# Kernel tuning notes

Measured on AMD Instinct MI355X. Metric: run time of the kernel, lower is better.

The kernel has to match this reference:

```python
import jax, jax.numpy as jnp
import numpy as np

N = 200000
H = 64
ARITIES = [2, 2, 3]
TUPLES = [300000, 300000, 200000]  # flat idx lengths = tuples * arity = 600000 each


def _linear_params(key, out_f, in_f, scale=0.05):
    kw, kb = jax.random.split(key)
    w = jax.random.normal(kw, (out_f, in_f), jnp.float32) * scale
    b = jax.random.normal(kb, (out_f,), jnp.float32) * scale
    return w, b


def setup_inputs() -> dict:
    key = jax.random.key(0)
    keys = jax.random.split(key, 16)
    inp = {}
    inp["node_states"] = jax.random.normal(keys[0], (N, H), jnp.float32)
    for r, (a, t) in enumerate(zip(ARITIES, TUPLES)):
        inp[f"rel{r}_idx"] = jax.random.randint(keys[1 + r], (t * a,), 0, N, jnp.int64)
    k = 4
    for r, a in enumerate(ARITIES):
        d = a * H
        w1, b1 = _linear_params(keys[k], d, d); k += 1
        w2, b2 = _linear_params(keys[k], d, d); k += 1
        inp[f"r{r}_w1"], inp[f"r{r}_b1"] = w1, b1
        inp[f"r{r}_w2"], inp[f"r{r}_b2"] = w2, b2
    inp["u_w1"], inp["u_b1"] = _linear_params(keys[k], 2 * H, 2 * H); k += 1
    inp["u_w2"], inp["u_b2"] = _linear_params(keys[k], H, 2 * H)
    return inp


def _forward(node_states, idxs, rel_params, u_w1, u_b1, u_w2, u_b2):
    outputs = []
    max_outputs = []
    for idx, a, (w1, b1, w2, b2) in zip(idxs, ARITIES, rel_params):
        # gather node rows, group by tuple: [T, a*H]
        x = node_states[idx].reshape(-1, a * H)
        h = jax.nn.relu(x @ w1.T + b1)
        o = (h @ w2.T + b2).reshape(-1, H)  # [T*a, H] message per participating node
        max_outputs.append(jnp.max(o))
        outputs.append((o, idx))
    max_offset = jnp.max(jnp.stack(max_outputs))
    exps_sum = jnp.full_like(node_states, 1e-16)
    for o, idx in outputs:
        exps_sum = exps_sum.at[idx].add(jnp.exp(8.0 * (o - max_offset)))
    max_msg = (1.0 / 8.0) * jnp.log(exps_sum) + max_offset  # smooth-max LSE
    cat = jnp.concatenate([max_msg, node_states], axis=1)
    h = jax.nn.relu(cat @ u_w1.T + u_b1)
    return h @ u_w2.T + u_b2


def reference(node_states, rel0_idx, rel1_idx, rel2_idx,
              r0_w1, r0_b1, r0_w2, r0_b2,
              r1_w1, r1_b1, r1_w2, r1_b2,
              r2_w1, r2_b1, r2_w2, r2_b2,
              u_w1, u_b1, u_w2, u_b2):
    idxs = [rel0_idx, rel1_idx, rel2_idx]
    rel_params = [(r0_w1, r0_b1, r0_w2, r0_b2),
                  (r1_w1, r1_b1, r1_w2, r1_b2),
                  (r2_w1, r2_b1, r2_w2, r2_b2)]
    return _forward(node_states, idxs, rel_params, u_w1, u_b1, u_w2, u_b2)
```

## Files before the change

kernel.cpp:

```cpp
#include <hip/hip_runtime.h>
#include <cstdint>

#define HD 64
#define NNODES 200000
#define NS_ELEMS (NNODES * HD)

typedef short bf8 __attribute__((ext_vector_type(8)));
typedef short s2v __attribute__((ext_vector_type(2)));
typedef float f32x4 __attribute__((ext_vector_type(4)));

__device__ __forceinline__ unsigned enc_f32(float f) {
    unsigned u = __float_as_uint(f);
    return (u & 0x80000000u) ? ~u : (u | 0x80000000u);
}
__device__ __forceinline__ float dec_f32(unsigned v) {
    return (v & 0x80000000u) ? __uint_as_float(v & 0x7fffffffu)
                             : __uint_as_float(~v);
}

__device__ __forceinline__ ushort f2bf(float f) {
    unsigned u = __float_as_uint(f);
    return (ushort)((u + 0x7fffu + ((u >> 16) & 1u)) >> 16);
}
__device__ __forceinline__ float bf2f(ushort b) {
    return __uint_as_float(((unsigned)b) << 16);
}

__device__ __forceinline__ void atom_pk_add_bf16(ushort* p, ushort lo, ushort hi) {
    s2v v; v[0] = (short)lo; v[1] = (short)hi;
#if __has_builtin(__builtin_amdgcn_flat_atomic_fadd_v2bf16)
    (void)__builtin_amdgcn_flat_atomic_fadd_v2bf16((s2v*)p, v);
#elif __has_builtin(__builtin_amdgcn_global_atomic_fadd_v2bf16)
    (void)__builtin_amdgcn_global_atomic_fadd_v2bf16(
        (__attribute__((address_space(1))) s2v*)p, v);
#else
    unsigned* a = (unsigned*)p;
    unsigned old = *a, assumed;
    do {
        assumed = old;
        float f0 = bf2f((ushort)(assumed & 0xffffu)) + bf2f(lo);
        float f1 = bf2f((ushort)(assumed >> 16))     + bf2f(hi);
        unsigned nv = (unsigned)f2bf(f0) | ((unsigned)f2bf(f1) << 16);
        old = atomicCAS(a, assumed, nv);
    } while (old != assumed);
#endif
}

struct PrepArgs {
    const float* src[8];
    ushort*      dst[8];
    int din[8], dout[8], nelem[8];
};

__global__ __launch_bounds__(256) void prep_kernel(
    const float* __restrict__ ns, ushort* __restrict__ ns16, PrepArgs pa, int total)
{
    int stride = gridDim.x * 256;
    for (int i = blockIdx.x * 256 + threadIdx.x; i < total; i += stride) {
        if (i < NS_ELEMS) { ns16[i] = f2bf(ns[i]); continue; }
        int e = i - NS_ELEMS;
        #pragma unroll
        for (int m = 0; m < 8; m++) {
            if (e < pa.nelem[m]) {
                int din = pa.din[m], dout = pa.dout[m];
                int n = e / din, k = e - n * din;
                pa.dst[m][(k >> 5) * dout * 32 + n * 32 + (k & 31)] = f2bf(pa.src[m][e]);
                e = 0x7fffffff;
            } else {
                e -= pa.nelem[m];
            }
        }
    }
}

__global__ __launch_bounds__(256) void hist_kernel(
    const int* __restrict__ i0, const int* __restrict__ i1, const int* __restrict__ i2,
    int b1e, int b2e, int total, int* __restrict__ cnt)
{
    int s = blockIdx.x * 256 + threadIdx.x;
    if (s >= total) return;
    int node = (s < b1e) ? i0[s] : (s < b2e ? i1[s - b1e] : i2[s - b2e]);
    atomicAdd(&cnt[node], 1);
}

__global__ __launch_bounds__(256) void scan1_kernel(
    const int* __restrict__ cnt, int* __restrict__ startv,
    int* __restrict__ partials, int n)
{
    __shared__ int wsum[4];
    int i = blockIdx.x * 256 + threadIdx.x;
    int v = (i < n) ? cnt[i] : 0;
    int lane = threadIdx.x & 63, wid = threadIdx.x >> 6;
    int x = v;
    #pragma unroll
    for (int off = 1; off < 64; off <<= 1) {
        int y = __shfl_up(x, off);
        if (lane >= off) x += y;
    }
    if (lane == 63) wsum[wid] = x;
    __syncthreads();
    int woff = 0;
    for (int w = 0; w < wid; w++) woff += wsum[w];
    int incl = x + woff;
    if (i < n) startv[i] = incl - v;
    if (threadIdx.x == 255) partials[blockIdx.x] = incl;
}

__global__ __launch_bounds__(1024) void scan2_kernel(int* __restrict__ partials, int nb)
{
    __shared__ int sh[1024];
    int t = threadIdx.x;
    int orig = (t < nb) ? partials[t] : 0;
    sh[t] = orig;
    __syncthreads();
    for (int off = 1; off < 1024; off <<= 1) {
        int v = (t >= off) ? sh[t - off] : 0;
        __syncthreads();
        sh[t] += v;
        __syncthreads();
    }
    if (t < nb) partials[t] = sh[t] - orig;
}

__global__ __launch_bounds__(256) void scan3_kernel(
    int* __restrict__ startv, int* __restrict__ offv,
    const int* __restrict__ partials, int n, int total)
{
    int i = blockIdx.x * 256 + threadIdx.x;
    if (i < n) {
        int s = startv[i] + partials[blockIdx.x];
        startv[i] = s;
        offv[i] = s;
    }
    if (i == 0) startv[n] = total;
}

__global__ __launch_bounds__(256) void fill_perm(
    const int* __restrict__ i0, const int* __restrict__ i1, const int* __restrict__ i2,
    int b1e, int b2e, int total, int* __restrict__ offv, int* __restrict__ perm)
{
    int s = blockIdx.x * 256 + threadIdx.x;
    if (s >= total) return;
    int node = (s < b1e) ? i0[s] : (s < b2e ? i1[s - b1e] : i2[s - b2e]);
    perm[s] = atomicAdd(&offv[node], 1);
}

template<int DIN, int DOUT, int NT, int PDIN>
__device__ __forceinline__ void mfma_layer(
    const ushort* __restrict__ WT, const float* __restrict__ bias,
    const ushort* __restrict__ Xs, int wave, int lane, f32x4 acc[2][NT])
{
    constexpr int KS = DIN / 32;
    const int q = lane >> 4, ln = lane & 15;
    const int n0 = wave * NT * 16;
    bf8 bf[NT][KS];
    #pragma unroll
    for (int nt = 0; nt < NT; nt++) {
        float bv = bias[n0 + nt * 16 + ln];
        acc[0][nt] = f32x4{bv, bv, bv, bv};
        acc[1][nt] = f32x4{bv, bv, bv, bv};
        #pragma unroll
        for (int ks = 0; ks < KS; ks++)
            bf[nt][ks] = *(const bf8*)(WT + (size_t)ks * DOUT * 32
                                          + (n0 + nt * 16 + ln) * 32 + q * 8);
    }
    #pragma unroll
    for (int mt = 0; mt < 2; mt++) {
        bf8 af[KS];
        #pragma unroll
        for (int ks = 0; ks < KS; ks++)
            af[ks] = *(const bf8*)(Xs + (mt * 16 + ln) * PDIN + ks * 32 + q * 8);
        #pragma unroll
        for (int ks = 0; ks < KS; ks++)
            #pragma unroll
            for (int nt = 0; nt < NT; nt++)
                acc[mt][nt] = __builtin_amdgcn_mfma_f32_16x16x32_bf16(
                    af[ks], bf[nt][ks], acc[mt][nt], 0, 0, 0);
    }
}

template<int A>
__global__ __launch_bounds__(256) void rel_mfma_pp(
    const ushort* __restrict__ ns16, const int* __restrict__ idx,
    const int* __restrict__ perm,
    const ushort* __restrict__ wt1, const float* __restrict__ b1,
    const ushort* __restrict__ wt2, const float* __restrict__ b2,
    ushort* __restrict__ O2, unsigned* __restrict__ Mword, int ntiles)
{
    constexpr int D  = A * HD;
    constexpr int PD = D + 8;
    constexpr int NT = D / 64;
    __shared__ __align__(16) ushort Xs[2][32 * PD];
    __shared__ __align__(16) ushort Hs[32 * PD];
    __shared__ int Pr[2][32 * A];
    __shared__ float wred[4];

    const int tid  = threadIdx.x;
    const int wave = tid >> 6, lane = tid & 63;
    const int q = lane >> 4, ln = lane & 15, n0 = wave * NT * 16;

    uint4 greg[A];
    int   pv = 0;
    float mblk = -3.0e38f;

    int ti = blockIdx.x;
    if (ti < ntiles) {
        int t0 = ti * 32;
        #pragma unroll
        for (int k = 0; k < A; k++) {
            int j = tid + k * 256;
            int slot = j >> 3, part = j & 7;
            int node = idx[t0 * A + slot];
            greg[k] = *(const uint4*)(ns16 + (size_t)node * HD + part * 8);
        }
        if (tid < 32 * A) pv = perm[t0 * A + tid];
        #pragma unroll
        for (int k = 0; k < A; k++) {
            int j = tid + k * 256;
            int slot = j >> 3, part = j & 7;
            int row = slot / A, sub = slot - row * A;
            *(uint4*)(&Xs[0][row * PD + sub * 64 + part * 8]) = greg[k];
        }
        if (tid < 32 * A) Pr[0][tid] = pv;
        __syncthreads();

        int cur = 0;
        for (;;) {
            int tn = ti + gridDim.x;
            bool has_next = tn < ntiles;
            if (has_next) {
                int t0n = tn * 32;
                #pragma unroll
                for (int k = 0; k < A; k++) {
                    int j = tid + k * 256;
                    int slot = j >> 3, part = j & 7;
                    int node = idx[t0n * A + slot];
                    greg[k] = *(const uint4*)(ns16 + (size_t)node * HD + part * 8);
                }
                if (tid < 32 * A) pv = perm[t0n * A + tid];
            }

            f32x4 acc[2][NT];
            mfma_layer<D, D, NT, PD>(wt1, b1, Xs[cur], wave, lane, acc);
            #pragma unroll
            for (int mt = 0; mt < 2; mt++)
                #pragma unroll
                for (int nt = 0; nt < NT; nt++)
                    #pragma unroll
                    for (int r = 0; r < 4; r++)
                        Hs[(mt * 16 + q * 4 + r) * PD + n0 + nt * 16 + ln] =
                            f2bf(fmaxf(acc[mt][nt][r], 0.f));
            __syncthreads();
            mfma_layer<D, D, NT, PD>(wt2, b2, Hs, wave, lane, acc);
            __syncthreads();

            #pragma unroll
            for (int mt = 0; mt < 2; mt++)
                #pragma unroll
                for (int nt = 0; nt < NT; nt++) {
                    int colg = n0 + nt * 16 + ln;
                    #pragma unroll
                    for (int r = 0; r < 4; r++) {
                        float o = acc[mt][nt][r];
                        mblk = fmaxf(mblk, o);
                        Hs[(mt * 16 + q * 4 + r) * PD + colg] = f2bf(__expf(8.f * o));
                    }
                }
            __syncthreads();

            #pragma unroll
            for (int k = 0; k < A; k++) {
                int j = tid + k * 256;
                int slot = j >> 3, part = j & 7;
                int row = slot / A, sub = slot - row * A;
                *(uint4*)(O2 + (size_t)Pr[cur][slot] * HD + part * 8) =
                    *(const uint4*)(&Hs[row * PD + sub * 64 + part * 8]);
            }

            if (!has_next) break;

            __syncthreads();
            int nxt = cur ^ 1;
            #pragma unroll
            for (int k = 0; k < A; k++) {
                int j = tid + k * 256;
                int slot = j >> 3, part = j & 7;
                int row = slot / A, sub = slot - row * A;
                *(uint4*)(&Xs[nxt][row * PD + sub * 64 + part * 8]) = greg[k];
            }
            if (tid < 32 * A) Pr[nxt][tid] = pv;
            __syncthreads();
            cur = nxt;
            ti = tn;
        }
    }

    #pragma unroll
    for (int off = 32; off; off >>= 1) mblk = fmaxf(mblk, __shfl_xor(mblk, off));
    if (lane == 0) wred[wave] = mblk;
    __syncthreads();
    if (tid == 0)
        atomicMax(Mword, enc_f32(fmaxf(fmaxf(wred[0], wred[1]),
                                       fmaxf(wred[2], wred[3]))));
}

template<int A>
__global__ __launch_bounds__(256) void rel_mfma(
    const ushort* __restrict__ ns16, const int* __restrict__ idx,
    const ushort* __restrict__ wt1, const float* __restrict__ b1,
    const ushort* __restrict__ wt2, const float* __restrict__ b2,
    ushort* __restrict__ S16, unsigned* __restrict__ Mword)
{
    constexpr int D  = A * HD;
    constexpr int PD = D + 8;
    constexpr int NT = D / 64;
    __shared__ __align__(16) ushort Xs[32 * PD];
    __shared__ __align__(16) ushort Hs[32 * PD];
    __shared__ int Is[32 * A];
    __shared__ float wred[4];

    const int tid = threadIdx.x;
    const int t0  = blockIdx.x * 32;

    if (tid < 32 * A) Is[tid] = idx[t0 * A + tid];
    for (int lin = tid; lin < 32 * A * 8; lin += 256) {
        int slot = lin >> 3, part = lin & 7;
        int node = idx[t0 * A + slot];
        int row = slot / A, sub = slot - row * A;
        *(uint4*)(Xs + row * PD + sub * 64 + part * 8) =
            *(const uint4*)(ns16 + (size_t)node * HD + part * 8);
    }
    __syncthreads();

    const int wave = tid >> 6, lane = tid & 63;
    const int q = lane >> 4, ln = lane & 15, n0 = wave * NT * 16;

    f32x4 acc[2][NT];
    mfma_layer<D, D, NT, PD>(wt1, b1, Xs, wave, lane, acc);
    #pragma unroll
    for (int mt = 0; mt < 2; mt++)
        #pragma unroll
        for (int nt = 0; nt < NT; nt++)
            #pragma unroll
            for (int r = 0; r < 4; r++)
                Hs[(mt * 16 + q * 4 + r) * PD + n0 + nt * 16 + ln] =
                    f2bf(fmaxf(acc[mt][nt][r], 0.f));
    __syncthreads();
    mfma_layer<D, D, NT, PD>(wt2, b2, Hs, wave, lane, acc);

    float m = -3.0e38f;
    const bool even = (ln & 1) == 0;
    #pragma unroll
    for (int mt = 0; mt < 2; mt++)
        #pragma unroll
        for (int nt = 0; nt < NT; nt++) {
            int colg = n0 + nt * 16 + ln;
            int sub  = colg >> 6;
            int featp = (colg & 63) & ~1;
            float e[4], p[4];
            #pragma unroll
            for (int r = 0; r < 4; r++) {
                float o = acc[mt][nt][r];
                m = fmaxf(m, o);
                e[r] = __expf(8.f * o);
            }
            #pragma unroll
            for (int r = 0; r < 4; r++) p[r] = __shfl_xor(e[r], 1);
            #pragma unroll
            for (int j = 0; j < 2; j++) {
                int r   = even ? j : (2 + j);
                int row = mt * 16 + q * 4 + r;
                int node = Is[row * A + sub];
                ushort lo = even ? f2bf(e[r]) : f2bf(p[r]);
                ushort hi = even ? f2bf(p[r]) : f2bf(e[r]);
                atom_pk_add_bf16(S16 + (size_t)node * HD + featp, lo, hi);
            }
        }
    #pragma unroll
    for (int off = 32; off; off >>= 1) m = fmaxf(m, __shfl_xor(m, off));
    if (lane == 0) wred[wave] = m;
    __syncthreads();
    if (tid == 0)
        atomicMax(Mword, enc_f32(fmaxf(fmaxf(wred[0], wred[1]),
                                       fmaxf(wred[2], wred[3]))));
}

__global__ __launch_bounds__(256) void update_lin(
    const float* __restrict__ ns, const ushort* __restrict__ O2,
    const int* __restrict__ startv,
    const unsigned* __restrict__ Mword,
    const ushort* __restrict__ wt1, const float* __restrict__ b1,
    const ushort* __restrict__ wt2, const float* __restrict__ b2,
    float* __restrict__ out)
{
    constexpr int D = 128, PD = D + 8;
    __shared__ __align__(16) ushort Xs[32 * PD];
    __shared__ __align__(16) ushort Hs[32 * PD];

    const int tid = threadIdx.x;
    const int r0  = blockIdx.x * 32;
    const float corr = 1e-16f * __expf(8.f * dec_f32(*Mword));

    for (int lin = tid; lin < 32 * 8; lin += 256) {
        int row = lin >> 3, p8 = (lin & 7) * 8;
        const float* src = ns + (size_t)(r0 + row) * HD + p8;
        float4 a = *(const float4*)src;
        float4 b = *(const float4*)(src + 4);
        ushort tmp[8] = { f2bf(a.x), f2bf(a.y), f2bf(a.z), f2bf(a.w),
                          f2bf(b.x), f2bf(b.y), f2bf(b.z), f2bf(b.w) };
        *(uint4*)(Xs + row * PD + 64 + p8) = *(uint4*)tmp;
    }

    {
        const int row = tid >> 3, f0 = (tid & 7) * 8;
        const int s0 = startv[r0 + row];
        const int s1 = startv[r0 + row + 1];
        float sum[8] = {0.f, 0.f, 0.f, 0.f, 0.f, 0.f, 0.f, 0.f};
        int k = s0;
        for (; k + 1 < s1; k += 2) {
            ushort ra[8], rb[8];
            *(uint4*)ra = *(const uint4*)(O2 + (size_t)k * HD + f0);
            *(uint4*)rb = *(const uint4*)(O2 + (size_t)(k + 1) * HD + f0);
            #pragma unroll
            for (int j = 0; j < 8; j++) sum[j] += bf2f(ra[j]) + bf2f(rb[j]);
        }
        if (k < s1) {
            ushort ra[8];
            *(uint4*)ra = *(const uint4*)(O2 + (size_t)k * HD + f0);
            #pragma unroll
            for (int j = 0; j < 8; j++) sum[j] += bf2f(ra[j]);
        }
        ushort tmp[8];
        #pragma unroll
        for (int j = 0; j < 8; j++)
            tmp[j] = f2bf(0.125f * __logf(sum[j] + corr));
        *(uint4*)(Xs + row * PD + f0) = *(uint4*)tmp;
    }
    __syncthreads();

    const int wave = tid >> 6, lane = tid & 63;
    const int q = lane >> 4, ln = lane & 15;

    f32x4 acc[2][2];
    mfma_layer<128, 128, 2, PD>(wt1, b1, Xs, wave, lane, acc);
    #pragma unroll
    for (int mt = 0; mt < 2; mt++)
        #pragma unroll
        for (int nt = 0; nt < 2; nt++)
            #pragma unroll
            for (int r = 0; r < 4; r++)
                Hs[(mt * 16 + q * 4 + r) * PD + wave * 32 + nt * 16 + ln] =
                    f2bf(fmaxf(acc[mt][nt][r], 0.f));
    __syncthreads();

    f32x4 acc2[2][1];
    mfma_layer<128, 64, 1, PD>(wt2, b2, Hs, wave, lane, acc2);
    #pragma unroll
    for (int mt = 0; mt < 2; mt++)
        #pragma unroll
        for (int r = 0; r < 4; r++)
            out[(size_t)(r0 + mt * 16 + q * 4 + r) * HD + wave * 16 + ln] =
                acc2[mt][0][r];
}

__global__ __launch_bounds__(256) void update_mfma(
    const float* __restrict__ ns, const ushort* __restrict__ S16,
    const unsigned* __restrict__ Mword,
    const ushort* __restrict__ wt1, const float* __restrict__ b1,
    const ushort* __restrict__ wt2, const float* __restrict__ b2,
    float* __restrict__ out)
{
    constexpr int D = 128, PD = D + 8;
    __shared__ __align__(16) ushort Xs[32 * PD];
    __shared__ __align__(16) ushort Hs[32 * PD];

    const int tid = threadIdx.x;
    const int r0  = blockIdx.x * 32;
    const float corr = 1e-16f * __expf(8.f * dec_f32(*Mword));

    for (int lin = tid; lin < 32 * 16; lin += 256) {
        int row = lin >> 4, c8 = (lin & 15) * 8;
        ushort tmp[8];
        if (c8 < 64) {
            ushort raw[8];
            *(uint4*)raw = *(const uint4*)(S16 + (size_t)(r0 + row) * HD + c8);
            #pragma unroll
            for (int j = 0; j < 8; j++)
                tmp[j] = f2bf(0.125f * __logf(bf2f(raw[j]) + corr));
        } else {
            #pragma unroll
            for (int j = 0; j < 8; j++)
                tmp[j] = f2bf(ns[(size_t)(r0 + row) * HD + (c8 - 64) + j]);
        }
        *(uint4*)(Xs + row * PD + c8) = *(uint4*)tmp;
    }
    __syncthreads();

    const int wave = tid >> 6, lane = tid & 63;
    const int q = lane >> 4, ln = lane & 15;

    f32x4 acc[2][2];
    mfma_layer<128, 128, 2, PD>(wt1, b1, Xs, wave, lane, acc);
    #pragma unroll
    for (int mt = 0; mt < 2; mt++)
        #pragma unroll
        for (int nt = 0; nt < 2; nt++)
            #pragma unroll
            for (int r = 0; r < 4; r++)
                Hs[(mt * 16 + q * 4 + r) * PD + wave * 32 + nt * 16 + ln] =
                    f2bf(fmaxf(acc[mt][nt][r], 0.f));
    __syncthreads();

    f32x4 acc2[2][1];
    mfma_layer<128, 64, 1, PD>(wt2, b2, Hs, wave, lane, acc2);
    #pragma unroll
    for (int mt = 0; mt < 2; mt++)
        #pragma unroll
        for (int r = 0; r < 4; r++)
            out[(size_t)(r0 + mt * 16 + q * 4 + r) * HD + wave * 16 + ln] =
                acc2[mt][0][r];
}

extern "C" void kernel_launch(void* const* d_in, const int* in_sizes, int n_in,
                              void* d_out, int out_size, void* d_ws, size_t ws_size,
                              hipStream_t stream)
{
    const float* ns   = (const float*)d_in[0];
    const int*   idx0 = (const int*)d_in[1];
    const int*   idx1 = (const int*)d_in[2];
    const int*   idx2 = (const int*)d_in[3];
    const float* W[8] = { (const float*)d_in[4],  (const float*)d_in[6],
                          (const float*)d_in[8],  (const float*)d_in[10],
                          (const float*)d_in[12], (const float*)d_in[14],
                          (const float*)d_in[16], (const float*)d_in[18] };
    const float* B[8] = { (const float*)d_in[5],  (const float*)d_in[7],
                          (const float*)d_in[9],  (const float*)d_in[11],
                          (const float*)d_in[13], (const float*)d_in[15],
                          (const float*)d_in[17], (const float*)d_in[19] };
    static const int DIN[8]  = {128,128,128,128,192,192,128,128};
    static const int DOUT[8] = {128,128,128,128,192,192,128, 64};

    const int n0f = in_sizes[1];
    const int n1f = in_sizes[2];
    const int n2f = in_sizes[3];
    const int TOT = n0f + n1f + n2f;
    const int T0 = n0f / 2, T1 = n1f / 2, T2 = n2f / 3;

    size_t wtot = 0;
    for (int m = 0; m < 8; m++) wtot += (size_t)DIN[m] * DOUT[m];

    size_t oO     = 0;
    size_t oNs    = oO  + (size_t)TOT * HD * 2;
    size_t oWT    = oNs + (size_t)NS_ELEMS * 2;
    size_t oPerm  = oWT + ((wtot * 2 + 255) & ~(size_t)255);
    size_t oStart = oPerm + (((size_t)TOT * 4 + 255) & ~(size_t)255);
    size_t oOff   = oStart + (((size_t)(NNODES + 1) * 4 + 255) & ~(size_t)255);
    size_t oPart  = oOff + (size_t)NNODES * 4;
    size_t oCnt   = oPart + 4096;
    size_t oMw    = oCnt + (size_t)NNODES * 4;
    size_t NEED   = oMw + 64;

    if (ws_size >= NEED) {
        ushort*   O2    = (ushort*)d_ws;
        ushort*   ns16  = (ushort*)((char*)d_ws + oNs);
        ushort*   WTb   = (ushort*)((char*)d_ws + oWT);
        int*      perm  = (int*)((char*)d_ws + oPerm);
        int*      start = (int*)((char*)d_ws + oStart);
        int*      offp  = (int*)((char*)d_ws + oOff);
        int*      part  = (int*)((char*)d_ws + oPart);
        int*      cnt   = (int*)((char*)d_ws + oCnt);
        unsigned* Mw    = (unsigned*)((char*)d_ws + oMw);

        PrepArgs pa;
        int total = NS_ELEMS;
        ushort* wt[8];
        {
            ushort* p = WTb;
            for (int m = 0; m < 8; m++) {
                pa.src[m] = W[m];
                pa.dst[m] = p;  wt[m] = p;
                pa.din[m] = DIN[m]; pa.dout[m] = DOUT[m];
                pa.nelem[m] = DIN[m] * DOUT[m];
                p += pa.nelem[m];
                total += pa.nelem[m];
            }
        }

        hipMemsetAsync((char*)d_ws + oCnt, 0, (size_t)NNODES * 4 + 64, stream);
        prep_kernel<<<4096, 256, 0, stream>>>(ns, ns16, pa, total);

        const int NB   = (NNODES + 255) / 256;
        const int gTOT = (TOT + 255) / 256;
        hist_kernel<<<gTOT, 256, 0, stream>>>(idx0, idx1, idx2, n0f, n0f + n1f, TOT, cnt);
        scan1_kernel<<<NB, 256, 0, stream>>>(cnt, start, part, NNODES);
        scan2_kernel<<<1, 1024, 0, stream>>>(part, NB);
        scan3_kernel<<<NB, 256, 0, stream>>>(start, offp, part, NNODES, TOT);
        fill_perm<<<gTOT, 256, 0, stream>>>(idx0, idx1, idx2, n0f, n0f + n1f, TOT, offp, perm);

        int nt0 = T0 / 32, nt1 = T1 / 32, nt2 = T2 / 32;
        int g2a = nt0 < 1536 ? nt0 : 1536;
        int g2b = nt1 < 1536 ? nt1 : 1536;
        int g3  = nt2 < 1024 ? nt2 : 1024;

        rel_mfma_pp<2><<<g2a, 256, 0, stream>>>(
            ns16, idx0, perm, wt[0], B[0], wt[1], B[1], O2, Mw, nt0);
        rel_mfma_pp<2><<<g2b, 256, 0, stream>>>(
            ns16, idx1, perm + n0f, wt[2], B[2], wt[3], B[3], O2, Mw, nt1);
        rel_mfma_pp<3><<<g3, 256, 0, stream>>>(
            ns16, idx2, perm + n0f + n1f, wt[4], B[4], wt[5], B[5], O2, Mw, nt2);

        update_lin<<<NNODES / 32, 256, 0, stream>>>(
            ns, O2, start, Mw, wt[6], B[6], wt[7], B[7], (float*)d_out);
    } else {
        ushort*   S16  = (ushort*)d_ws;
        size_t    offM = (size_t)NNODES * HD * sizeof(ushort);
        unsigned* Mw   = (unsigned*)((char*)d_ws + offM);
        ushort*   ns16 = (ushort*)((char*)d_ws + offM + 64);
        ushort*   WTb  = ns16 + (size_t)NS_ELEMS;

        PrepArgs pa;
        int total = NS_ELEMS;
        ushort* wt[8];
        {
            ushort* p = WTb;
            for (int m = 0; m < 8; m++) {
                pa.src[m] = W[m];
                pa.dst[m] = p;  wt[m] = p;
                pa.din[m] = DIN[m]; pa.dout[m] = DOUT[m];
                pa.nelem[m] = DIN[m] * DOUT[m];
                p += pa.nelem[m];
                total += pa.nelem[m];
            }
        }

        hipMemsetAsync(d_ws, 0, offM + 64, stream);
        prep_kernel<<<4096, 256, 0, stream>>>(ns, ns16, pa, total);

        rel_mfma<2><<<T0 / 32, 256, 0, stream>>>(ns16, idx0, wt[0], B[0], wt[1], B[1], S16, Mw);
        rel_mfma<2><<<T1 / 32, 256, 0, stream>>>(ns16, idx1, wt[2], B[2], wt[3], B[3], S16, Mw);
        rel_mfma<3><<<T2 / 32, 256, 0, stream>>>(ns16, idx2, wt[4], B[4], wt[5], B[5], S16, Mw);
        update_mfma<<<NNODES / 32, 256, 0, stream>>>(ns, S16, Mw, wt[6], B[6], wt[7], B[7],
                                                     (float*)d_out);
    }
}
```

Before: 576.3 us.

## Restructure MFMA layer to hold A fragments in registers and stream weights

Adds a new MFMA layer routine that loads both M-tiles of activation fragments from LDS once, then walks the K dimension while prefetching the next weight fragments, instead of holding all weight fragments for every K step in registers. It also adds a min-blocks-per-CU launch bound of 4, removes a barrier before the next-tile LDS write, and lowers the grid cap for the arity-2 relations. The aim is to cut register pressure and raise occupancy while still overlapping weight loads with MFMA work. Weights are now reloaded per tile from global/L2 in a more serial pattern, and dropping the barrier relies on the preceding barrier to keep the Xs buffer swap correct.

After: 667.0 us. 15.7% more time.

```diff
diff --git a/kernel.cpp b/kernel.cpp
--- a/kernel.cpp
+++ b/kernel.cpp
@@ -179,8 +179,57 @@
     }
 }
 
+template<int DIN, int DOUT, int NT, int PDIN>
+__device__ __forceinline__ void mfma_layer_lr(
+    const ushort* __restrict__ WT, const float* __restrict__ bias,
+    const ushort* __restrict__ Xs, int wave, int lane, f32x4 acc[2][NT])
+{
+    constexpr int KS = DIN / 32;
+    const int q = lane >> 4, ln = lane & 15;
+    const int n0 = wave * NT * 16;
+
+    bf8 af[2][KS];
+    #pragma unroll
+    for (int mt = 0; mt < 2; mt++)
+        #pragma unroll
+        for (int ks = 0; ks < KS; ks++)
+            af[mt][ks] = *(const bf8*)(Xs + (mt * 16 + ln) * PDIN + ks * 32 + q * 8);
+
+    #pragma unroll
+    for (int nt = 0; nt < NT; nt++) {
+        float bv = bias[n0 + nt * 16 + ln];
+        acc[0][nt] = f32x4{bv, bv, bv, bv};
+        acc[1][nt] = f32x4{bv, bv, bv, bv};
+    }
+
+    const ushort* wp = WT + (size_t)(n0 + ln) * 32 + q * 8;
+    bf8 bc[NT], bn[NT];
+    #pragma unroll
+    for (int nt = 0; nt < NT; nt++)
+        bc[nt] = *(const bf8*)(wp + nt * 16 * 32);
+    #pragma unroll
+    for (int ks = 0; ks < KS; ks++) {
+        if (ks + 1 < KS) {
+            #pragma unroll
+            for (int nt = 0; nt < NT; nt++)
+                bn[nt] = *(const bf8*)(wp + (size_t)(ks + 1) * DOUT * 32 + nt * 16 * 32);
+        }
+        #pragma unroll
+        for (int nt = 0; nt < NT; nt++) {
+            acc[0][nt] = __builtin_amdgcn_mfma_f32_16x16x32_bf16(
+                af[0][ks], bc[nt], acc[0][nt], 0, 0, 0);
+            acc[1][nt] = __builtin_amdgcn_mfma_f32_16x16x32_bf16(
+                af[1][ks], bc[nt], acc[1][nt], 0, 0, 0);
+        }
+        if (ks + 1 < KS) {
+            #pragma unroll
+            for (int nt = 0; nt < NT; nt++) bc[nt] = bn[nt];
+        }
+    }
+}
+
 template<int A>
-__global__ __launch_bounds__(256) void rel_mfma_pp(
+__global__ __launch_bounds__(256, 4) void rel_mfma_pp(
     const ushort* __restrict__ ns16, const int* __restrict__ idx,
     const int* __restrict__ perm,
     const ushort* __restrict__ wt1, const float* __restrict__ b1,
@@ -241,7 +290,7 @@
             }
 
             f32x4 acc[2][NT];
-            mfma_layer<D, D, NT, PD>(wt1, b1, Xs[cur], wave, lane, acc);
+            mfma_layer_lr<D, D, NT, PD>(wt1, b1, Xs[cur], wave, lane, acc);
             #pragma unroll
             for (int mt = 0; mt < 2; mt++)
                 #pragma unroll
@@ -251,7 +300,7 @@
                         Hs[(mt * 16 + q * 4 + r) * PD + n0 + nt * 16 + ln] =
                             f2bf(fmaxf(acc[mt][nt][r], 0.f));
             __syncthreads();
-            mfma_layer<D, D, NT, PD>(wt2, b2, Hs, wave, lane, acc);
+            mfma_layer_lr<D, D, NT, PD>(wt2, b2, Hs, wave, lane, acc);
             __syncthreads();
 
             #pragma unroll
@@ -279,7 +328,6 @@
 
             if (!has_next) break;
 
-            __syncthreads();
             int nxt = cur ^ 1;
             #pragma unroll
             for (int k = 0; k < A; k++) {
@@ -598,8 +646,8 @@
         fill_perm<<<gTOT, 256, 0, stream>>>(idx0, idx1, idx2, n0f, n0f + n1f, TOT, offp, perm);
 
         int nt0 = T0 / 32, nt1 = T1 / 32, nt2 = T2 / 32;
-        int g2a = nt0 < 1536 ? nt0 : 1536;
-        int g2b = nt1 < 1536 ? nt1 : 1536;
+        int g2a = nt0 < 1024 ? nt0 : 1024;
+        int g2b = nt1 < 1024 ? nt1 : 1024;
         int g3  = nt2 < 1024 ? nt2 : 1024;
 
         rel_mfma_pp<2><<<g2a, 256, 0, stream>>>(
```
